# Kernel tuning notes

Measured on AMD Instinct MI355X. Metric: run time of the kernel, lower is better.

## Reference

```python
import jax, jax.numpy as jnp
import numpy as np
from jax import lax

EPS = 1e-5

def conv2d(x, w, pad):
    # x: NCHW, w: OIHW
    return lax.conv_general_dilated(x, w, (1, 1), [(pad, pad), (pad, pad)],
                                    dimension_numbers=('NCHW', 'OIHW', 'NCHW'))

def batchnorm(x, gamma, beta):
    # training-mode BN: batch statistics over N,H,W (biased variance, as torch)
    m = jnp.mean(x, axis=(0, 2, 3), keepdims=True)
    v = jnp.var(x, axis=(0, 2, 3), keepdims=True)
    g = gamma.reshape(1, -1, 1, 1)
    b = beta.reshape(1, -1, 1, 1)
    return (x - m) * jax.lax.rsqrt(v + EPS) * g + b

def setup_inputs() -> dict:
    key = jax.random.key(0)
    ks = jax.random.split(key, 8)
    B, Cin, Cmid, NC, H, W = 4, 2048, 512, 19, 64, 64
    s = lambda fan: (2.0 / fan) ** 0.5
    return {
        'x':  jax.random.normal(ks[0], (B, Cin, H, W), jnp.float32),
        'Wa': jax.random.normal(ks[1], (Cmid, Cin, 3, 3), jnp.float32) * s(Cin * 9),
        'ga': jnp.ones((Cmid,), jnp.float32),
        'ba': jnp.zeros((Cmid,), jnp.float32),
        'Wb': jax.random.normal(ks[2], (Cmid, Cmid, 1, 1), jnp.float32) * s(Cmid),
        'bb': jnp.zeros((Cmid,), jnp.float32),
        'W1': jax.random.normal(ks[3], (Cmid, Cin + Cmid, 3, 3), jnp.float32) * s((Cin + Cmid) * 9),
        'g1': jnp.ones((Cmid,), jnp.float32),
        'b1': jnp.zeros((Cmid,), jnp.float32),
        'W4': jax.random.normal(ks[4], (NC, Cmid, 1, 1), jnp.float32) * s(Cmid),
        'b4': jnp.zeros((NC,), jnp.float32),
    }

def reference(x, Wa, ga, ba, Wb, bb, W1, g1, b1, W4, b4):
    # conva: 3x3 conv (no bias) -> BN -> ReLU
    out = jax.nn.relu(batchnorm(conv2d(x, Wa, 1), ga, ba))
    # convb: 1x1 conv with bias
    out = conv2d(out, Wb, 0) + bb.reshape(1, -1, 1, 1)
    # concat input with projected features along channels
    out = jnp.concatenate([x, out], axis=1)  # [B, Cin+Cmid, H, W]
    # b1 (3x3, no bias) -> b2 BN -> b3 ReLU
    out = jax.nn.relu(batchnorm(conv2d(out, W1, 1), g1, b1))
    # b4: 1x1 classifier conv with bias
    out_final = conv2d(out, W4, 0) + b4.reshape(1, -1, 1, 1)
    return (out, out_final)
```

## Files before the change

kernel.cpp:

```cpp
#include <hip/hip_runtime.h>

typedef unsigned short ushort_t;
typedef unsigned int uint_t;
typedef unsigned long long ulong_t;

typedef __bf16 bf16x8 __attribute__((ext_vector_type(8)));
typedef float f32x4 __attribute__((ext_vector_type(4)));
typedef float f32x16 __attribute__((ext_vector_type(16)));
typedef unsigned short u16x4 __attribute__((ext_vector_type(4)));

#define DEV __device__ __forceinline__
#define SB() __builtin_amdgcn_sched_barrier(0)
#define WAITV(n) asm volatile("s_waitcnt vmcnt(" #n ")" ::: "memory")

DEV ushort_t f2bf(float x) {
  uint_t u = __float_as_uint(x);
  u += 0x7fffu + ((u >> 16) & 1u);
  return (ushort_t)(u >> 16);
}
DEV float bf2f(ushort_t h) { return __uint_as_float(((uint_t)h) << 16); }

DEV void gload16(ulong_t g, const void* l) {
  __builtin_amdgcn_global_load_lds(
      (__attribute__((address_space(1))) void*)g,
      (__attribute__((address_space(3))) void*)(void*)l,
      16, 0, 0);
}
DEV int nxt3(int x) { return x == 2 ? 0 : x + 1; }

__global__ void zero_k(float* __restrict__ p, int n) {
  int i = blockIdx.x * 256 + threadIdx.x;
  if (i < n) p[i] = 0.f;
}

__global__ __launch_bounds__(256) void cvt_x_k(const float* __restrict__ X,
                                               ushort_t* __restrict__ P) {
  __shared__ float T[64][65];
  const int t = threadIdx.x;
  const int p0 = blockIdx.x * 64;
  const int c0 = blockIdx.y * 64;
  const int b = p0 >> 12;
  const int pin0 = p0 & 4095;
#pragma unroll
  for (int it = 0; it < 4; ++it) {
    const int cl = it * 16 + (t >> 4);
    const int pl = (t & 15) * 4;
    const f32x4 v = *(const f32x4*)&X[((size_t)(b * 2048 + c0 + cl)) * 4096 + pin0 + pl];
#pragma unroll
    for (int j = 0; j < 4; ++j) T[cl][pl + j] = v[j];
  }
  __syncthreads();
#pragma unroll
  for (int it = 0; it < 4; ++it) {
    const int pl = it * 16 + (t >> 4);
    const int cl = (t & 15) * 4;
    u16x4 h, l;
#pragma unroll
    for (int j = 0; j < 4; ++j) {
      float v = T[cl + j][pl];
      ushort_t hh = f2bf(v);
      h[j] = hh;
      l[j] = f2bf(v - bf2f(hh));
    }
    const int c = c0 + cl;
    const size_t o = (size_t)(p0 + pl) * 4096 + (size_t)((c >> 5) << 6) + (c & 31);
    *(u16x4*)&P[o] = h;
    *(u16x4*)&P[o + 32] = l;
  }
}

__global__ __launch_bounds__(256) void cvt_w3_k(const float* __restrict__ W,
                                                ushort_t* __restrict__ P,
                                                int I, int O) {
  const int t = threadIdx.x;
  const int o = blockIdx.y;
  const int i = blockIdx.x * 256 + t;
  const float* src = W + ((size_t)o * I + i) * 9;
  float v[9];
#pragma unroll
  for (int j = 0; j < 9; ++j) v[j] = src[j];
#pragma unroll
  for (int j = 0; j < 9; ++j) {
    ushort_t h = f2bf(v[j]);
    const size_t d = (size_t)(j * O + o) * (I * 2) + (size_t)((i >> 5) << 6) + (i & 31);
    P[d] = h;
    P[d + 32] = f2bf(v[j] - bf2f(h));
  }
}

__global__ __launch_bounds__(256) void cvt_e_k(const float* __restrict__ W,
                                               ushort_t* __restrict__ P) {
  int i = blockIdx.x * 256 + threadIdx.x;
  float v = W[i];
  ushort_t h = f2bf(v);
  const int o = i >> 9, ic = i & 511;
  const size_t d = (size_t)o * 1024 + (size_t)((ic >> 5) << 6) + (ic & 31);
  P[d] = h;
  P[d + 32] = f2bf(v - bf2f(h));
}

__global__ __launch_bounds__(256) void stats_k(const float* __restrict__ X,
                                               float* __restrict__ S,
                                               float* __restrict__ Q) {
  const int t = threadIdx.x;
  const int r0 = blockIdx.x * 32;
  const int c = t * 2;
  float s0 = 0, s1 = 0, q0 = 0, q1 = 0;
  for (int r = 0; r < 32; ++r) {
    const float2 v = *(const float2*)&X[((size_t)(r0 + r)) * 512 + c];
    s0 += v.x; s1 += v.y;
    q0 += v.x * v.x; q1 += v.y * v.y;
  }
  atomicAdd(&S[c], s0); atomicAdd(&S[c + 1], s1);
  atomicAdd(&Q[c], q0); atomicAdd(&Q[c + 1], q1);
}

__global__ void bnparams_k(const float* __restrict__ S, const float* __restrict__ Q,
                           const float* __restrict__ g, const float* __restrict__ b,
                           float* __restrict__ sc, float* __restrict__ sh) {
  const int t = threadIdx.x;
  const float m = S[t] * (1.0f / 16384.0f);
  const float v = Q[t] * (1.0f / 16384.0f) - m * m;
  const float inv = rsqrtf(v + 1e-5f);
  const float s = g[t] * inv;
  sc[t] = s;
  sh[t] = b[t] - m * s;
}

__global__ __launch_bounds__(256) void bnact_k(const float* __restrict__ X,
                                               const float* __restrict__ sc,
                                               const float* __restrict__ sh,
                                               ushort_t* __restrict__ P) {
  const size_t i0 = ((size_t)blockIdx.x * 256 + threadIdx.x) * 16;
  const int c0 = (int)(i0 & 511);
  const size_t px = i0 >> 9;
#pragma unroll
  for (int q = 0; q < 4; ++q) {
    const f32x4 v = *(const f32x4*)&X[i0 + q * 4];
    const f32x4 s = *(const f32x4*)&sc[c0 + q * 4];
    const f32x4 d = *(const f32x4*)&sh[c0 + q * 4];
    u16x4 h, l;
#pragma unroll
    for (int j = 0; j < 4; ++j) {
      float y = fmaf(v[j], s[j], d[j]);
      y = fmaxf(y, 0.f);
      ushort_t hh = f2bf(y);
      h[j] = hh;
      l[j] = f2bf(y - bf2f(hh));
    }
    const int c = c0 + q * 4;
    const size_t o = px * 1024 + (size_t)((c >> 5) << 6) + (c & 31);
    *(u16x4*)&P[o] = h;
    *(u16x4*)&P[o + 32] = l;
  }
}

__global__ __launch_bounds__(256) void bn_nchw_k(const float* __restrict__ X,
                                                 const float* __restrict__ sc,
                                                 const float* __restrict__ sh,
                                                 float* __restrict__ O) {
  __shared__ float T[64][65];
  const int t = threadIdx.x;
  const int p0 = blockIdx.x * 64;
  const int c0 = blockIdx.y * 64;
  const int b = p0 >> 12, pin0 = p0 & 4095;
#pragma unroll
  for (int it = 0; it < 4; ++it) {
    const int pl = it * 16 + (t >> 4);
    const int cl = (t & 15) * 4;
    const f32x4 v = *(const f32x4*)&X[((size_t)(p0 + pl)) * 512 + c0 + cl];
#pragma unroll
    for (int j = 0; j < 4; ++j) {
      float y = fmaf(v[j], sc[c0 + cl + j], sh[c0 + cl + j]);
      T[pl][cl + j] = fmaxf(y, 0.f);
    }
  }
  __syncthreads();
#pragma unroll
  for (int it = 0; it < 4; ++it) {
    const int cl = it * 16 + (t >> 4);
    const int pl = (t & 15) * 4;
    f32x4 o;
#pragma unroll
    for (int j = 0; j < 4; ++j) o[j] = T[pl + j][cl];
    *(f32x4*)&O[((size_t)(b * 512 + c0 + cl)) * 4096 + pin0 + pl] = o;
  }
}

__global__ __launch_bounds__(256) void conv4_k(const float* __restrict__ X,
                                               const float* __restrict__ sc,
                                               const float* __restrict__ sh,
                                               const float* __restrict__ W4,
                                               const float* __restrict__ B4,
                                               float* __restrict__ O) {
  __shared__ float A[256][69];
  __shared__ float WL[64][19];
  const int t = threadIdx.x;
  const int g0 = blockIdx.x * 256;
  float acc[19];
#pragma unroll
  for (int n = 0; n < 19; ++n) acc[n] = 0.f;
  for (int kc = 0; kc < 8; ++kc) {
    const int k0 = kc * 64;
    __syncthreads();
#pragma unroll
    for (int it = 0; it < 16; ++it) {
      const int rl = it * 16 + (t >> 4);
      const int cl = (t & 15) * 4;
      const f32x4 v = *(const f32x4*)&X[((size_t)(g0 + rl)) * 512 + k0 + cl];
#pragma unroll
      for (int j = 0; j < 4; ++j)
        A[rl][cl + j] = fmaxf(fmaf(v[j], sc[k0 + cl + j], sh[k0 + cl + j]), 0.f);
    }
    for (int e = t; e < 1216; e += 256) {
      int k = e / 19, n = e - k * 19;
      WL[k][n] = W4[(size_t)n * 512 + k0 + k];
    }
    __syncthreads();
#pragma unroll 8
    for (int k = 0; k < 64; ++k) {
      const float a = A[t][k];
#pragma unroll
      for (int n = 0; n < 19; ++n) acc[n] = fmaf(a, WL[k][n], acc[n]);
    }
  }
  const int g = g0 + t;
  const int b = g >> 12, pin = g & 4095;
#pragma unroll
  for (int n = 0; n < 19; ++n)
    O[((size_t)(b * 19 + n)) * 4096 + pin] = acc[n] + B4[n];
}

template <int TAPS, int EPI>
__global__ __launch_bounds__(512, 2) void conv_k(
    const ushort_t* __restrict__ A1, int S1, int CB1,
    const ushort_t* __restrict__ A2, int S2, int CB2,
    const ushort_t* __restrict__ WB, int CBt,
    const ushort_t* __restrict__ zp,
    float* __restrict__ Co, ushort_t* __restrict__ Cp,
    const float* __restrict__ bias) {
  constexpr int RW = (TAPS == 9) ? 6 : 4;
  constexpr int AJ = RW * 4;
  constexpr int AI = (2 * AJ) / 8;
  constexpr int APL = AJ * 1024;
  constexpr int ABUF = 2 * APL;
  constexpr int HO = (TAPS == 9) ? 64 : 0;
  __shared__ char lds_all[163840];
  char* Ald = lds_all;
  char* Bld = lds_all + 98304;
  const int t = threadIdx.x, lane = t & 63, wid = t >> 6;
  const int wr = wid >> 1, wc = wid & 1;
  const int gid = blockIdx.x, xcd = gid & 7, k_ = gid >> 3;
  const int by = xcd * 8 + (k_ & 7), bx = k_ >> 3;
  const int b = by >> 4, r0 = (by & 15) * 4, bbase = b * 4096;
  const int gsrc = ((lane & 3) - ((lane >> 3) & 3)) & 3;
  const int NBS = CBt * 64;

  auto stageA = [&](int cb, int bufA) {
#pragma unroll
    for (int i = 0; i < AI; ++i) {
      const int idx = wid * AI + i;
      const int d = idx / AJ, j = idx - d * AJ;
      const int irow = r0 + (j >> 2) - ((TAPS == 9) ? 1 : 0);
      int cbl = cb;
      const ushort_t* base = A1;
      int S = S1;
      if (CB2 > 0 && cbl >= CB1) { base = A2; S = S2; cbl -= CB1; }
      const int gpx = bbase + irow * 64 + (j & 3) * 16 + (lane >> 2);
      const ulong_t el = (ulong_t)gpx * (uint_t)S + (uint_t)(cbl * 64 + d * 32 + gsrc * 8);
      const bool oob = (unsigned)irow >= 64u;
      const ulong_t src = oob ? (ulong_t)(zp + lane * 8) : (ulong_t)(base + el);
      gload16(src, Ald + bufA + (d * AJ + j) * 1024);
    }
  };
  auto stageB = [&](int cb, int tapIdx, int bufB) {
#pragma unroll
    for (int q = 0; q < 2; ++q) {
      const int s = wid * 2 + q;
      const int d = s >> 3, r = s & 7, nb = r >> 1, h = r & 1;
      const int co = bx * 128 + nb * 32 + h * 16 + (lane >> 2);
      const ulong_t el = (ulong_t)(tapIdx * 512 + co) * (uint_t)NBS +
                         (uint_t)(cb * 64 + d * 32 + gsrc * 8);
      gload16((ulong_t)(WB + el), Bld + bufB + s * 1024);
    }
  };

  f32x16 acc[2][2];
#pragma unroll
  for (int i = 0; i < 2; ++i)
#pragma unroll
    for (int j2 = 0; j2 < 2; ++j2) acc[i][j2] = (f32x16){0.f};

  const int pxl = lane & 31;
  const int khalf = lane >> 5;
  const int rotB = (pxl >> 1) & 3;
  int boff[2][2];
#pragma unroll
  for (int ni = 0; ni < 2; ++ni)
#pragma unroll
    for (int kk = 0; kk < 2; ++kk) {
      const int pos = (kk * 2 + khalf + rotB) & 3;
      boff[ni][kk] = (wc * 2 + ni) * 2048 + pxl * 64 + pos * 16;
    }

  auto compute = [&](int abufB, int bbufB, int ro, int dx) {
    const char* Ab = Ald + abufB;
    const char* Bb = Bld + bbufB;
    bf16x8 a[2][2][2], bf[2][2][2];
#pragma unroll
    for (int mi = 0; mi < 2; ++mi)
#pragma unroll
      for (int kk = 0; kk < 2; ++kk) {
        int px = wr * 64 + mi * 32 + pxl + ro;
        px = px < 0 ? 0 : (px > RW * 64 - 1 ? RW * 64 - 1 : px);
        const int pos = (kk * 2 + khalf + (px >> 1)) & 3;
        const int ao = px * 64 + pos * 16;
        a[mi][kk][0] = *(const bf16x8*)(Ab + ao);
        a[mi][kk][1] = *(const bf16x8*)(Ab + APL + ao);
      }
#pragma unroll
    for (int ni = 0; ni < 2; ++ni)
#pragma unroll
      for (int kk = 0; kk < 2; ++kk) {
        bf[ni][kk][0] = *(const bf16x8*)(Bb + boff[ni][kk]);
        bf[ni][kk][1] = *(const bf16x8*)(Bb + 8192 + boff[ni][kk]);
      }
    if (TAPS == 9) {
      if (dx == -1 && pxl == 0) {
        bf16x8 z = {};
        a[0][0][0] = z; a[0][0][1] = z; a[0][1][0] = z; a[0][1][1] = z;
      }
      if (dx == 1 && pxl == 31) {
        bf16x8 z = {};
        a[1][0][0] = z; a[1][0][1] = z; a[1][1][0] = z; a[1][1][1] = z;
      }
    }
    __builtin_amdgcn_s_setprio(1);
#pragma unroll
    for (int kk = 0; kk < 2; ++kk)
#pragma unroll
      for (int mi = 0; mi < 2; ++mi)
#pragma unroll
        for (int ni = 0; ni < 2; ++ni) {
          acc[mi][ni] = __builtin_amdgcn_mfma_f32_32x32x16_bf16(
              a[mi][kk][0], bf[ni][kk][0], acc[mi][ni], 0, 0, 0);
          acc[mi][ni] = __builtin_amdgcn_mfma_f32_32x32x16_bf16(
              a[mi][kk][0], bf[ni][kk][1], acc[mi][ni], 0, 0, 0);
          acc[mi][ni] = __builtin_amdgcn_mfma_f32_32x32x16_bf16(
              a[mi][kk][1], bf[ni][kk][0], acc[mi][ni], 0, 0, 0);
        }
    __builtin_amdgcn_s_setprio(0);
  };

  if constexpr (TAPS == 9) {
    const int NT = CBt * 9;
    stageA(0, 0);
    stageB(0, 0, 0);
    stageB(0, 1, 16384);
    SB();
    for (int T = 0; T < NT; T += 2) {
      WAITV(0);
      SB();
      __builtin_amdgcn_s_barrier();
      SB();
      const int T2 = T + 2, T3 = T + 3;
      if (T2 < NT) {
        const int cs2 = T2 / 9, tp2 = T2 - cs2 * 9;
        if (tp2 == 0) stageA(cs2, (cs2 & 1) * ABUF);
        stageB(cs2, tp2, (T2 & 3) * 16384);
      }
      if (T3 < NT) {
        const int cs3 = T3 / 9, tp3 = T3 - cs3 * 9;
        if (tp3 == 0) stageA(cs3, (cs3 & 1) * ABUF);
        stageB(cs3, tp3, (T3 & 3) * 16384);
      }
      SB();
      {
        const int cs = T / 9, tap = T - cs * 9;
        const int dy = tap / 3 - 1, dx = tap - (tap / 3) * 3 - 1;
        compute((cs & 1) * ABUF, (T & 3) * 16384, HO + dy * 64 + dx, dx);
      }
      {
        const int T1 = T + 1;
        const int cs = T1 / 9, tap = T1 - cs * 9;
        const int dy = tap / 3 - 1, dx = tap - (tap / 3) * 3 - 1;
        compute((cs & 1) * ABUF, (T1 & 3) * 16384, HO + dy * 64 + dx, dx);
      }
    }
  } else {
    int rr = 0;
    stageA(0, 0); SB();
    stageB(0, 0, 0); SB();
    stageA(1, ABUF); SB();
    stageB(1, 0, 16384); SB();
    for (int cs = 0; cs < CBt; ++cs) {
      SB();
      WAITV(6);
      SB();
      __builtin_amdgcn_s_barrier();
      SB();
      const int rr2 = nxt3(nxt3(rr));
      stageA(cs + 2, rr2 * ABUF);
      stageB(cs + 2, 0, rr2 * 16384);
      SB();
      compute(rr * ABUF, rr * 16384, 0, 0);
      rr = nxt3(rr);
    }
  }

  const int row0 = by * 256 + wr * 64;
  const int col0 = bx * 128 + wc * 64;
  const int rb = 4 * khalf;
  if (EPI == 0) {
#pragma unroll
    for (int mi = 0; mi < 2; ++mi)
#pragma unroll
      for (int ni = 0; ni < 2; ++ni) {
        const int c = col0 + ni * 32 + pxl;
#pragma unroll
        for (int rg = 0; rg < 16; ++rg) {
          const int r = row0 + mi * 32 + (rg & 3) + 8 * (rg >> 2) + rb;
          Co[(size_t)r * 512 + c] = acc[mi][ni][rg];
        }
      }
  } else {
#pragma unroll
    for (int ni = 0; ni < 2; ++ni) {
      const int c = col0 + ni * 32 + pxl;
      const float bv = bias[c];
      const size_t cg = (size_t)((c >> 5) << 6) + (c & 31);
#pragma unroll
      for (int mi = 0; mi < 2; ++mi)
#pragma unroll
        for (int rg = 0; rg < 16; ++rg) {
          const int r = row0 + mi * 32 + (rg & 3) + 8 * (rg >> 2) + rb;
          const float v = acc[mi][ni][rg] + bv;
          const ushort_t h = f2bf(v);
          Cp[(size_t)r * 1024 + cg] = h;
          Cp[(size_t)r * 1024 + cg + 32] = f2bf(v - bf2f(h));
        }
    }
  }
}

extern "C" void kernel_launch(void* const* d_in, const int* in_sizes, int n_in,
                              void* d_out, int out_size, void* d_ws, size_t ws_size,
                              hipStream_t stream) {
  const float* x  = (const float*)d_in[0];
  const float* Wa = (const float*)d_in[1];
  const float* ga = (const float*)d_in[2];
  const float* ba = (const float*)d_in[3];
  const float* Wb = (const float*)d_in[4];
  const float* bb = (const float*)d_in[5];
  const float* W1 = (const float*)d_in[6];
  const float* g1 = (const float*)d_in[7];
  const float* b1 = (const float*)d_in[8];
  const float* W4 = (const float*)d_in[9];
  const float* b4 = (const float*)d_in[10];
  float* out0 = (float*)d_out;
  float* outF = out0 + (size_t)4 * 512 * 64 * 64;

  char* ws = (char*)d_ws;
  size_t off = 0;
  auto take = [&](size_t bytes) -> char* {
    char* p = ws + off;
    off += (bytes + 255) & ~(size_t)255;
    return p;
  };
  const size_t PAD = 16384;
  ushort_t* zp  = (ushort_t*)take(8192);
  float* sumA = (float*)take(2048);
  float* ssA  = (float*)take(2048);
  float* scA  = (float*)take(2048);
  float* shA  = (float*)take(2048);
  float* sum1 = (float*)take(2048);
  float* ss1  = (float*)take(2048);
  float* sc1  = (float*)take(2048);
  float* sh1  = (float*)take(2048);
  ushort_t* X2  = (ushort_t*)take((size_t)16384 * 4096 * 2 + PAD);
  ushort_t* WA2 = (ushort_t*)take((size_t)9 * 512 * 4096 * 2 + PAD);
  ushort_t* W12 = (ushort_t*)take((size_t)9 * 512 * 5120 * 2 + PAD);
  ushort_t* WBb = (ushort_t*)take((size_t)512 * 1024 * 2 + PAD);
  ushort_t* oA2 = (ushort_t*)take((size_t)16384 * 1024 * 2 + PAD);
  ushort_t* oB2 = (ushort_t*)take((size_t)16384 * 1024 * 2 + PAD);
  float* convaRaw = (float*)take((size_t)16384 * 512 * 4);
  float* conv1Raw = (float*)take((size_t)16384 * 512 * 4);
  if (ws_size < off) return;

  zero_k<<<dim3(24), dim3(256), 0, stream>>>((float*)ws, 6144);
  cvt_x_k<<<dim3(256, 32), dim3(256), 0, stream>>>(x, X2);
  cvt_w3_k<<<dim3(8, 512), dim3(256), 0, stream>>>(Wa, WA2, 2048, 512);
  cvt_w3_k<<<dim3(10, 512), dim3(256), 0, stream>>>(W1, W12, 2560, 512);
  cvt_e_k<<<dim3(1024), dim3(256), 0, stream>>>(Wb, WBb);

  conv_k<9, 0><<<dim3(256), dim3(512), 0, stream>>>(
      X2, 4096, 64, X2, 4096, 0, WA2, 64, zp, convaRaw, nullptr, nullptr);
  stats_k<<<dim3(512), dim3(256), 0, stream>>>(convaRaw, sumA, ssA);
  bnparams_k<<<dim3(1), dim3(512), 0, stream>>>(sumA, ssA, ga, ba, scA, shA);
  bnact_k<<<dim3(2048), dim3(256), 0, stream>>>(convaRaw, scA, shA, oA2);

  conv_k<1, 1><<<dim3(256), dim3(512), 0, stream>>>(
      oA2, 1024, 18, oA2, 1024, 0, WBb, 16, zp, nullptr, oB2, bb);

  conv_k<9, 0><<<dim3(256), dim3(512), 0, stream>>>(
      X2, 4096, 64, oB2, 1024, 16, W12, 80, zp, conv1Raw, nullptr, nullptr);
  stats_k<<<dim3(512), dim3(256), 0, stream>>>(conv1Raw, sum1, ss1);
  bnparams_k<<<dim3(1), dim3(512), 0, stream>>>(sum1, ss1, g1, b1, sc1, sh1);

  bn_nchw_k<<<dim3(256, 8), dim3(256), 0, stream>>>(conv1Raw, sc1, sh1, out0);
  conv4_k<<<dim3(64), dim3(256), 0, stream>>>(conv1Raw, sc1, sh1, W4, b4, outF);
}
```

Before: 1.979 ms.

## Store LDS tiles in MFMA-fragment order and interleave staging with compute

```diff
diff --git a/kernel.cpp b/kernel.cpp
--- a/kernel.cpp
+++ b/kernel.cpp
@@ -240,11 +240,11 @@
     float* __restrict__ Co, ushort_t* __restrict__ Cp,
     const float* __restrict__ bias) {
   constexpr int RW = (TAPS == 9) ? 6 : 4;
-  constexpr int AJ = RW * 4;
-  constexpr int AI = (2 * AJ) / 8;
-  constexpr int APL = AJ * 1024;
+  constexpr int PB = RW * 2;
+  constexpr int SPD = PB * 2;
+  constexpr int AI = (2 * SPD) / 8;
+  constexpr int APL = SPD * 1024;
   constexpr int ABUF = 2 * APL;
-  constexpr int HO = (TAPS == 9) ? 64 : 0;
   __shared__ char lds_all[163840];
   char* Ald = lds_all;
   char* Bld = lds_all + 98304;
@@ -253,35 +253,40 @@
   const int gid = blockIdx.x, xcd = gid & 7, k_ = gid >> 3;
   const int by = xcd * 8 + (k_ & 7), bx = k_ >> 3;
   const int b = by >> 4, r0 = (by & 15) * 4, bbase = b * 4096;
-  const int gsrc = ((lane & 3) - ((lane >> 3) & 3)) & 3;
+  const int pxl = lane & 31;
+  const int khalf = lane >> 5;
+  const int lofs = lane * 16;
   const int NBS = CBt * 64;
 
   auto stageA = [&](int cb, int bufA) {
 #pragma unroll
     for (int i = 0; i < AI; ++i) {
-      const int idx = wid * AI + i;
-      const int d = idx / AJ, j = idx - d * AJ;
-      const int irow = r0 + (j >> 2) - ((TAPS == 9) ? 1 : 0);
+      const int g = wid * AI + i;
+      const int d = g / SPD, rem = g - d * SPD;
+      const int pxb = rem >> 1, kk = rem & 1;
+      const int p = pxb * 32 + pxl;
+      const int irow = r0 + (p >> 6) - ((TAPS == 9) ? 1 : 0);
       int cbl = cb;
       const ushort_t* base = A1;
       int S = S1;
       if (CB2 > 0 && cbl >= CB1) { base = A2; S = S2; cbl -= CB1; }
-      const int gpx = bbase + irow * 64 + (j & 3) * 16 + (lane >> 2);
-      const ulong_t el = (ulong_t)gpx * (uint_t)S + (uint_t)(cbl * 64 + d * 32 + gsrc * 8);
+      const int gpx = bbase + irow * 64 + (p & 63);
+      const ulong_t el = (ulong_t)gpx * (uint_t)S +
+                         (uint_t)(cbl * 64 + d * 32 + (kk * 2 + khalf) * 8);
       const bool oob = (unsigned)irow >= 64u;
       const ulong_t src = oob ? (ulong_t)(zp + lane * 8) : (ulong_t)(base + el);
-      gload16(src, Ald + bufA + (d * AJ + j) * 1024);
+      gload16(src, Ald + bufA + d * APL + (pxb * 2 + kk) * 1024);
     }
   };
   auto stageB = [&](int cb, int tapIdx, int bufB) {
 #pragma unroll
     for (int q = 0; q < 2; ++q) {
       const int s = wid * 2 + q;
-      const int d = s >> 3, r = s & 7, nb = r >> 1, h = r & 1;
-      const int co = bx * 128 + nb * 32 + h * 16 + (lane >> 2);
+      const int d = s >> 3, rem = s & 7, cob = rem >> 1, kk = rem & 1;
+      const int co = bx * 128 + cob * 32 + pxl;
       const ulong_t el = (ulong_t)(tapIdx * 512 + co) * (uint_t)NBS +
-                         (uint_t)(cb * 64 + d * 32 + gsrc * 8);
-      gload16((ulong_t)(WB + el), Bld + bufB + s * 1024);
+                         (uint_t)(cb * 64 + d * 32 + (kk * 2 + khalf) * 8);
+      gload16((ulong_t)(WB + el), Bld + bufB + d * 8192 + (cob * 2 + kk) * 1024);
     }
   };
 
@@ -291,40 +296,36 @@
 #pragma unroll
     for (int j2 = 0; j2 < 2; ++j2) acc[i][j2] = (f32x16){0.f};
 
-  const int pxl = lane & 31;
-  const int khalf = lane >> 5;
-  const int rotB = (pxl >> 1) & 3;
-  int boff[2][2];
-#pragma unroll
-  for (int ni = 0; ni < 2; ++ni)
-#pragma unroll
-    for (int kk = 0; kk < 2; ++kk) {
-      const int pos = (kk * 2 + khalf + rotB) & 3;
-      boff[ni][kk] = (wc * 2 + ni) * 2048 + pxl * 64 + pos * 16;
-    }
-
-  auto compute = [&](int abufB, int bbufB, int ro, int dx) {
+  auto compute = [&](int abufB, int bbufB, int prow, int dx) {
     const char* Ab = Ald + abufB;
     const char* Bb = Bld + bbufB;
     bf16x8 a[2][2][2], bf[2][2][2];
 #pragma unroll
-    for (int mi = 0; mi < 2; ++mi)
+    for (int ni = 0; ni < 2; ++ni)
 #pragma unroll
       for (int kk = 0; kk < 2; ++kk) {
-        int px = wr * 64 + mi * 32 + pxl + ro;
+        const int bo = (wc * 2 + ni) * 2048 + kk * 1024 + lofs;
+        bf[ni][kk][0] = *(const bf16x8*)(Bb + bo);
+        bf[ni][kk][1] = *(const bf16x8*)(Bb + 8192 + bo);
+      }
+#pragma unroll
+    for (int mi = 0; mi < 2; ++mi) {
+      const int pb0 = prow * 2 + mi;
+      int ao0;
+      if (dx == 0) {
+        ao0 = pb0 * 2048 + lofs;
+      } else {
+        int px = pb0 * 32 + pxl + dx;
         px = px < 0 ? 0 : (px > RW * 64 - 1 ? RW * 64 - 1 : px);
-        const int pos = (kk * 2 + khalf + (px >> 1)) & 3;
-        const int ao = px * 64 + pos * 16;
+        ao0 = (px >> 5) * 2048 + khalf * 512 + (px & 31) * 16;
+      }
+#pragma unroll
+      for (int kk = 0; kk < 2; ++kk) {
+        const int ao = ao0 + kk * 1024;
         a[mi][kk][0] = *(const bf16x8*)(Ab + ao);
         a[mi][kk][1] = *(const bf16x8*)(Ab + APL + ao);
       }
-#pragma unroll
-    for (int ni = 0; ni < 2; ++ni)
-#pragma unroll
-      for (int kk = 0; kk < 2; ++kk) {
-        bf[ni][kk][0] = *(const bf16x8*)(Bb + boff[ni][kk]);
-        bf[ni][kk][1] = *(const bf16x8*)(Bb + 8192 + boff[ni][kk]);
-      }
+    }
     if (TAPS == 9) {
       if (dx == -1 && pxl == 0) {
         bf16x8 z = {};
@@ -337,18 +338,26 @@
     }
     __builtin_amdgcn_s_setprio(1);
 #pragma unroll
-    for (int kk = 0; kk < 2; ++kk)
+    for (int kk = 0; kk < 2; ++kk) {
 #pragma unroll
       for (int mi = 0; mi < 2; ++mi)
 #pragma unroll
-        for (int ni = 0; ni < 2; ++ni) {
+        for (int ni = 0; ni < 2; ++ni)
           acc[mi][ni] = __builtin_amdgcn_mfma_f32_32x32x16_bf16(
               a[mi][kk][0], bf[ni][kk][0], acc[mi][ni], 0, 0, 0);
+#pragma unroll
+      for (int mi = 0; mi < 2; ++mi)
+#pragma unroll
+        for (int ni = 0; ni < 2; ++ni)
           acc[mi][ni] = __builtin_amdgcn_mfma_f32_32x32x16_bf16(
               a[mi][kk][0], bf[ni][kk][1], acc[mi][ni], 0, 0, 0);
+#pragma unroll
+      for (int mi = 0; mi < 2; ++mi)
+#pragma unroll
+        for (int ni = 0; ni < 2; ++ni)
           acc[mi][ni] = __builtin_amdgcn_mfma_f32_32x32x16_bf16(
               a[mi][kk][1], bf[ni][kk][0], acc[mi][ni], 0, 0, 0);
-        }
+    }
     __builtin_amdgcn_s_setprio(0);
   };
 
@@ -363,12 +372,19 @@
       SB();
       __builtin_amdgcn_s_barrier();
       SB();
-      const int T2 = T + 2, T3 = T + 3;
+      const int T2 = T + 2;
       if (T2 < NT) {
         const int cs2 = T2 / 9, tp2 = T2 - cs2 * 9;
         if (tp2 == 0) stageA(cs2, (cs2 & 1) * ABUF);
         stageB(cs2, tp2, (T2 & 3) * 16384);
       }
+      SB();
+      {
+        const int cs = T / 9, tap = T - cs * 9;
+        compute((cs & 1) * ABUF, (T & 3) * 16384, wr + tap / 3, tap % 3 - 1);
+      }
+      SB();
+      const int T3 = T + 3;
       if (T3 < NT) {
         const int cs3 = T3 / 9, tp3 = T3 - cs3 * 9;
         if (tp3 == 0) stageA(cs3, (cs3 & 1) * ABUF);
@@ -376,15 +392,9 @@
       }
       SB();
       {
-        const int cs = T / 9, tap = T - cs * 9;
-        const int dy = tap / 3 - 1, dx = tap - (tap / 3) * 3 - 1;
-        compute((cs & 1) * ABUF, (T & 3) * 16384, HO + dy * 64 + dx, dx);
-      }
-      {
         const int T1 = T + 1;
         const int cs = T1 / 9, tap = T1 - cs * 9;
-        const int dy = tap / 3 - 1, dx = tap - (tap / 3) * 3 - 1;
-        compute((cs & 1) * ABUF, (T1 & 3) * 16384, HO + dy * 64 + dx, dx);
+        compute((cs & 1) * ABUF, (T1 & 3) * 16384, wr + tap / 3, tap % 3 - 1);
       }
     }
   } else {
@@ -403,7 +413,7 @@
       stageA(cs + 2, rr2 * ABUF);
       stageB(cs + 2, 0, rr2 * 16384);
       SB();
-      compute(rr * ABUF, rr * 16384, 0, 0);
+      compute(rr * ABUF, rr * 16384, wr, 0);
       rr = nxt3(rr);
     }
   }
```

Result: no change. 1.997 ms (+0.9%).
